# Kernel optimization log

Measured on AMD Instinct MI355X. Metric: run time of the kernel, lower is better.

The kernel has to match this reference:

```python
import jax, jax.numpy as jnp
import numpy as np
from jax import lax

B, T, E, K = 64, 512, 2048, 32


def setup_inputs() -> dict:
    key = jax.random.key(0)
    ks = jax.random.split(key, 8)
    X = jax.random.normal(ks[0], (B, T, E), dtype=jnp.float32)
    y = jax.random.randint(ks[1], (B, T), 0, K, dtype=jnp.int32)
    # variable-length mask: lengths in [T//2, T], position 0 always valid
    lengths = jax.random.randint(ks[2], (B,), T // 2, T + 1)
    mask = (jnp.arange(T)[None, :] < lengths[:, None])
    W = jax.random.normal(ks[3], (E, K), dtype=jnp.float32) * 0.02
    b = jnp.zeros((K,), dtype=jnp.float32)
    transitions = jax.random.normal(ks[4], (K, K), dtype=jnp.float32) * 0.1
    start_transitions = jax.random.normal(ks[5], (K,), dtype=jnp.float32) * 0.1
    end_transitions = jax.random.normal(ks[6], (K,), dtype=jnp.float32) * 0.1
    return {"X": X, "y": y, "mask": mask, "W": W, "b": b,
            "transitions": transitions,
            "start_transitions": start_transitions,
            "end_transitions": end_transitions}


def _input_likelihood(logits, mask, trans, start, end):
    # forward algorithm (log partition), AllenNLP semantics
    lt = jnp.transpose(logits, (1, 0, 2))  # [T,B,K]
    mt = mask.T                            # [T,B]
    alpha0 = start[None, :] + lt[0]        # [B,K]

    def step(alpha, xm):
        x, m = xm  # x:[B,K], m:[B]
        inner = alpha[:, :, None] + trans[None, :, :] + x[:, None, :]  # [B,K,K]
        new = jax.nn.logsumexp(inner, axis=1)
        return jnp.where(m[:, None], new, alpha), None

    alpha, _ = lax.scan(step, alpha0, (lt[1:], mt[1:]))
    return jax.nn.logsumexp(alpha + end[None, :], axis=1)  # [B]


def _joint_likelihood(logits, tags, mask, trans, start, end):
    maskf = mask.astype(logits.dtype)
    emit = jnp.take_along_axis(logits, tags[:, :, None], axis=2)[:, :, 0]  # [B,T]
    emit_score = jnp.sum(emit * maskf, axis=1)
    trans_sc = trans[tags[:, :-1], tags[:, 1:]]  # [B,T-1]
    trans_score = jnp.sum(trans_sc * maskf[:, 1:], axis=1)
    lengths = jnp.sum(mask.astype(jnp.int32), axis=1)
    last_tags = jnp.take_along_axis(tags, (lengths - 1)[:, None], axis=1)[:, 0]
    return start[tags[:, 0]] + emit_score + trans_score + end[last_tags]


def reference(X, y, mask, W, b, transitions, start_transitions, end_transitions):
    logits = jnp.einsum('bte,ek->btk', X, W) + b  # projection
    log_num = _joint_likelihood(logits, y, mask, transitions,
                                start_transitions, end_transitions)
    log_den = _input_likelihood(logits, mask, transitions,
                                start_transitions, end_transitions)
    # CRF.forward training path: loss = -crf(inputs, tags, mask)
    return -jnp.sum(log_num - log_den)
```

## Files before the change

### kernel.cpp

```cpp
#include <hip/hip_runtime.h>

#define Bn 64
#define Tn 512
#define En 2048
#define Kn 32
#define Mn (Bn*Tn)
#define LOG2E 1.4426950408889634f
#define LN2   0.6931471805599453f
#define NSEG 8
#define SEGLEN 64

typedef __attribute__((ext_vector_type(8)))  short short8;
typedef __attribute__((ext_vector_type(4)))  float floatx4;
typedef __attribute__((ext_vector_type(16))) float floatx16;

__device__ inline unsigned int pack_bf16(float a, float b) {
    unsigned int ua = __float_as_uint(a), ub = __float_as_uint(b);
    return ((ua + 0x8000u) >> 16) | (((ub + 0x8000u) & 0xFFFF0000u));
}
__device__ inline unsigned int pack_trunc(float lo, float hi) {
    return (__float_as_uint(lo) >> 16) | (__float_as_uint(hi) & 0xFFFF0000u);
}
__device__ inline float rdlane(float v, int l) {
    return __uint_as_float(__builtin_amdgcn_readlane(__float_as_uint(v), l));
}

__global__ __launch_bounds__(256) void prep_kernel(const float* __restrict__ W,
                                                   unsigned short* __restrict__ Wt,
                                                   float* __restrict__ out) {
    int idx = blockIdx.x * 256 + threadIdx.x;
    int k = idx >> 11, e = idx & 2047;
    float w = W[e * Kn + k];
    Wt[idx] = (unsigned short)((__float_as_uint(w) + 0x8000u) >> 16);
    if (idx == 0) out[0] = 0.f;
}

__global__ __launch_bounds__(256) void gemm_kernel(const float* __restrict__ X,
                                                   const float* __restrict__ bias,
                                                   const unsigned short* __restrict__ Wt,
                                                   float* __restrict__ logits2) {
    const int tid  = threadIdx.x;
    const int wave = tid >> 6;
    const int lane = tid & 63;
    const int ml   = lane & 15;
    const int quad = lane >> 4;
    const int row0 = blockIdx.x * 64;

    const float*          xp  = X  + (size_t)(row0 + wave * 16 + ml) * En + quad * 8;
    const unsigned short* b0p = Wt + ml * En        + quad * 8;
    const unsigned short* b1p = Wt + (16 + ml) * En + quad * 8;

    floatx4 acc0 = {0.f,0.f,0.f,0.f};
    floatx4 acc1 = {0.f,0.f,0.f,0.f};

    #pragma unroll 8
    for (int e0 = 0; e0 < En; e0 += 32) {
        float4 xa = *(const float4*)(xp + e0);
        float4 xb = *(const float4*)(xp + e0 + 4);
        short8 b0 = *(const short8*)(b0p + e0);
        short8 b1 = *(const short8*)(b1p + e0);
        union { unsigned int u[4]; short8 s; } av;
        av.u[0] = pack_bf16(xa.x, xa.y);
        av.u[1] = pack_bf16(xa.z, xa.w);
        av.u[2] = pack_bf16(xb.x, xb.y);
        av.u[3] = pack_bf16(xb.z, xb.w);
        acc0 = __builtin_amdgcn_mfma_f32_16x16x32_bf16(av.s, b0, acc0, 0, 0, 0);
        acc1 = __builtin_amdgcn_mfma_f32_16x16x32_bf16(av.s, b1, acc1, 0, 0, 0);
    }

    const float bc0 = bias[ml], bc1 = bias[16 + ml];
    const int gr = row0 + wave * 16 + quad * 4;
    #pragma unroll
    for (int r = 0; r < 4; ++r) {
        logits2[(size_t)(gr + r) * Kn + ml]      = (acc0[r] + bc0) * LOG2E;
        logits2[(size_t)(gr + r) * Kn + 16 + ml] = (acc1[r] + bc1) * LOG2E;
    }
}

__device__ inline int seq_len(const void* maskp, int b, int lane) {
    unsigned int first = *(const unsigned int*)maskp;
    int mode = (first <= 1u) ? 0 : (first == 0x3F800000u ? 2 : 1);
    int len = 0;
    if (mode == 0) {
        const int* mb = (const int*)maskp + b * Tn;
        for (int t = lane; t < Tn; t += 64) len += (mb[t] != 0);
    } else if (mode == 1) {
        const unsigned char* mb = (const unsigned char*)maskp + b * Tn;
        for (int t = lane; t < Tn; t += 64) len += (mb[t] != 0);
    } else {
        const float* mb = (const float*)maskp + b * Tn;
        for (int t = lane; t < Tn; t += 64) len += (mb[t] != 0.f);
    }
    #pragma unroll
    for (int o = 32; o; o >>= 1) len += __shfl_xor(len, o, 64);
    return len;
}

__global__ __launch_bounds__(64) void crf_seg_kernel(const float* __restrict__ logits2,
                                                     const void* __restrict__ maskp,
                                                     const float* __restrict__ trans,
                                                     float* __restrict__ Hs,
                                                     float* __restrict__ Ss) {
    const int bx = blockIdx.x;
    const int b = bx >> 3, s = bx & 7;
    const int lane = threadIdx.x;
    const int j = lane & 31;
    const int h = lane >> 5;

    const int len = seq_len(maskp, b, lane);
    if (s * SEGLEN >= len) return;
    const int tstart = (s == 0) ? 1 : s * SEGLEN;
    const int tend   = min(s * SEGLEN + SEGLEN - 1, len - 1);

    float PT1[8], PT2[8];
    #pragma unroll
    for (int i = 0; i < 8; ++i) {
        PT1[i] = __builtin_exp2f(trans[(8 * h + i) * Kn + j] * LOG2E);
        PT2[i] = __builtin_exp2f(trans[(16 + 8 * h + i) * Kn + j] * LOG2E);
    }

    union U4 { unsigned int u[4]; short8 v; };
    U4 fb1, fb2;
    #pragma unroll
    for (int p = 0; p < 4; ++p) { fb1.u[p] = 0u; fb2.u[p] = 0u; }
    int i1 = j - 8 * h;
    if (i1 >= 0 && i1 < 8) fb1.u[i1 >> 1] |= 0x3F80u << (16 * (i1 & 1));
    int i2 = j - 16 - 8 * h;
    if (i2 >= 0 && i2 < 8) fb2.u[i2 >> 1] |= 0x3F80u << (16 * (i2 & 1));

    const float* xrow = logits2 + (size_t)b * Tn * Kn + j;
    floatx16 Hc;
    float S = 0.f;
    int stepc = 0;

    float cur[4], nxt[4];
    #pragma unroll
    for (int q = 0; q < 4; ++q) cur[q] = xrow[min(tstart + q, tend) * Kn];

    for (int g = tstart; g <= tend; g += 4) {
        #pragma unroll
        for (int q = 0; q < 4; ++q) nxt[q] = xrow[min(g + 4 + q, tend) * Kn];
        #pragma unroll
        for (int q = 0; q < 4; ++q) {
            if (g + q <= tend) {
                float e = __builtin_exp2f(cur[q]);
                U4 fa1, fa2;
                #pragma unroll
                for (int p = 0; p < 4; ++p) {
                    fa1.u[p] = pack_trunc(e * PT1[2 * p], e * PT1[2 * p + 1]);
                    fa2.u[p] = pack_trunc(e * PT2[2 * p], e * PT2[2 * p + 1]);
                }
                floatx16 acc = {0.f,0.f,0.f,0.f,0.f,0.f,0.f,0.f,
                                0.f,0.f,0.f,0.f,0.f,0.f,0.f,0.f};
                acc = __builtin_amdgcn_mfma_f32_32x32x16_bf16(fa1.v, fb1.v, acc, 0, 0, 0);
                acc = __builtin_amdgcn_mfma_f32_32x32x16_bf16(fa2.v, fb2.v, acc, 0, 0, 0);

                if ((stepc & 7) == 7) {
                    float m = acc[0];
                    #pragma unroll
                    for (int r = 1; r < 16; ++r) m = fmaxf(m, acc[r]);
                    #pragma unroll
                    for (int o = 1; o < 64; o <<= 1) m = fmaxf(m, __shfl_xor(m, o, 64));
                    int eb = (int)((__float_as_uint(m) >> 23) & 0xFF);
                    float scale = __uint_as_float((unsigned int)(254 - eb) << 23);
                    #pragma unroll
                    for (int r = 0; r < 16; ++r) acc[r] *= scale;
                    S += (float)(eb - 127);
                }
                ++stepc;
                Hc = acc;

                unsigned int w[8], pw[8];
                #pragma unroll
                for (int p = 0; p < 8; ++p) w[p] = pack_trunc(acc[2 * p], acc[2 * p + 1]);
                #pragma unroll
                for (int p = 0; p < 8; ++p) pw[p] = __shfl_xor(w[p], 32, 64);
                if (h == 0) {
                    fb1.u[0] = w[0];  fb1.u[1] = w[1];  fb1.u[2] = pw[0]; fb1.u[3] = pw[1];
                    fb2.u[0] = w[4];  fb2.u[1] = w[5];  fb2.u[2] = pw[4]; fb2.u[3] = pw[5];
                } else {
                    fb1.u[0] = pw[2]; fb1.u[1] = pw[3]; fb1.u[2] = w[2];  fb1.u[3] = w[3];
                    fb2.u[0] = pw[6]; fb2.u[1] = pw[7]; fb2.u[2] = w[6];  fb2.u[3] = w[7];
                }
            }
        }
        #pragma unroll
        for (int q = 0; q < 4; ++q) cur[q] = nxt[q];
    }

    float* hp = Hs + (size_t)(b * 8 + s) * 1024;
    #pragma unroll
    for (int r = 0; r < 16; ++r) {
        int row = (r & 3) + 8 * (r >> 2) + 4 * h;
        hp[row * 32 + j] = Hc[r];
    }
    if (lane == 0) Ss[b * 8 + s] = S;
}

__global__ __launch_bounds__(64) void crf_comb_kernel(const float* __restrict__ logits2,
                                                      const int* __restrict__ y,
                                                      const void* __restrict__ maskp,
                                                      const float* __restrict__ trans,
                                                      const float* __restrict__ start,
                                                      const float* __restrict__ endt,
                                                      const float* __restrict__ Hs,
                                                      const float* __restrict__ Ss,
                                                      float* __restrict__ out) {
    const int b = blockIdx.x;
    const int lane = threadIdx.x;
    const int j = lane & 31;

    const int len = seq_len(maskp, b, lane);

    const int* yb = y + b * Tn;
    float num2 = 0.f;
    for (int t = lane; t < Tn; t += 64) {
        if (t < len) {
            int yt = yb[t];
            num2 += logits2[((size_t)b * Tn + t) * Kn + yt];
            if (t >= 1) num2 += trans[yb[t - 1] * Kn + yt] * LOG2E;
        }
    }
    if (lane == 0) num2 += (start[yb[0]] + endt[yb[len - 1]]) * LOG2E;
    #pragma unroll
    for (int o = 32; o; o >>= 1) num2 += __shfl_xor(num2, o, 64);

    float a2 = start[j] * LOG2E + logits2[(size_t)b * Tn * Kn + j];
    float m0 = a2;
    #pragma unroll
    for (int o = 1; o < 64; o <<= 1) m0 = fmaxf(m0, __shfl_xor(m0, o, 64));
    float S = m0;
    float u = __builtin_exp2f(a2 - m0);

    for (int s = 0; s < NSEG; ++s) {
        if (s * SEGLEN >= len) break;
        const float* hrow = Hs + (size_t)(b * 8 + s) * 1024 + j * 32;
        float4 hr[8];
        #pragma unroll
        for (int p = 0; p < 8; ++p) hr[p] = *(const float4*)(hrow + 4 * p);
        float v0 = 0.f, v1 = 0.f, v2 = 0.f, v3 = 0.f;
        #pragma unroll
        for (int p = 0; p < 8; ++p) {
            v0 = fmaf(hr[p].x, rdlane(u, 4 * p),     v0);
            v1 = fmaf(hr[p].y, rdlane(u, 4 * p + 1), v1);
            v2 = fmaf(hr[p].z, rdlane(u, 4 * p + 2), v2);
            v3 = fmaf(hr[p].w, rdlane(u, 4 * p + 3), v3);
        }
        float v = (v0 + v1) + (v2 + v3);
        float mm = v;
        #pragma unroll
        for (int o = 1; o < 64; o <<= 1) mm = fmaxf(mm, __shfl_xor(mm, o, 64));
        int eb = (int)((__float_as_uint(mm) >> 23) & 0xFF);
        u = v * __uint_as_float((unsigned int)(254 - eb) << 23);
        S += (float)(eb - 127) + Ss[b * 8 + s];
    }

    float fv = (lane < 32) ? u * __builtin_exp2f(endt[j] * LOG2E) : 0.f;
    #pragma unroll
    for (int o = 32; o; o >>= 1) fv += __shfl_xor(fv, o, 64);
    float den2 = S + __builtin_log2f(fv);

    if (lane == 0) atomicAdd(out, (den2 - num2) * LN2);
}

extern "C" void kernel_launch(void* const* d_in, const int* in_sizes, int n_in,
                              void* d_out, int out_size, void* d_ws, size_t ws_size,
                              hipStream_t stream) {
    const float* X     = (const float*)d_in[0];
    const int*   y     = (const int*)  d_in[1];
    const void*  mask  =               d_in[2];
    const float* W     = (const float*)d_in[3];
    const float* bias  = (const float*)d_in[4];
    const float* trans = (const float*)d_in[5];
    const float* start = (const float*)d_in[6];
    const float* endt  = (const float*)d_in[7];
    float* out = (float*)d_out;

    char* ws = (char*)d_ws;
    float*          logits2 = (float*)ws;                         ws += (size_t)Mn * Kn * 4;
    unsigned short* Wt      = (unsigned short*)ws;                ws += (size_t)Kn * En * 2;
    float*          Hs      = (float*)ws;                         ws += (size_t)Bn * NSEG * 1024 * 4;
    float*          Ss      = (float*)ws;

    prep_kernel<<<256, 256, 0, stream>>>(W, Wt, out);
    gemm_kernel<<<Mn / 64, 256, 0, stream>>>(X, bias, Wt, logits2);
    crf_seg_kernel<<<Bn * NSEG, 64, 0, stream>>>(logits2, mask, trans, Hs, Ss);
    crf_comb_kernel<<<Bn, 64, 0, stream>>>(logits2, y, mask, trans, start, endt, Hs, Ss, out);
}
```

Baseline: 431.9 us.

## Fuse projection GEMM with per-segment CRF forward scan via shared-memory logits

Merges the GEMM kernel and the segmented CRF forward kernel into one launch. Each 64-row GEMM block maps to exactly one (batch, segment) pair, keeps its logits tile in LDS, and wave 0 then runs the segment recurrence from LDS instead of rereading global memory. This removes a kernel launch and the global round-trip for the scan inputs. The cost is that the serial scan now runs on only one wave of a 256-thread block while the other waves sit idle, which may reduce GEMM occupancy or lengthen the block's tail.

```diff
diff --git a/kernel.cpp b/kernel.cpp
--- a/kernel.cpp
+++ b/kernel.cpp
@@ -33,48 +33,6 @@
     float w = W[e * Kn + k];
     Wt[idx] = (unsigned short)((__float_as_uint(w) + 0x8000u) >> 16);
     if (idx == 0) out[0] = 0.f;
-}
-
-__global__ __launch_bounds__(256) void gemm_kernel(const float* __restrict__ X,
-                                                   const float* __restrict__ bias,
-                                                   const unsigned short* __restrict__ Wt,
-                                                   float* __restrict__ logits2) {
-    const int tid  = threadIdx.x;
-    const int wave = tid >> 6;
-    const int lane = tid & 63;
-    const int ml   = lane & 15;
-    const int quad = lane >> 4;
-    const int row0 = blockIdx.x * 64;
-
-    const float*          xp  = X  + (size_t)(row0 + wave * 16 + ml) * En + quad * 8;
-    const unsigned short* b0p = Wt + ml * En        + quad * 8;
-    const unsigned short* b1p = Wt + (16 + ml) * En + quad * 8;
-
-    floatx4 acc0 = {0.f,0.f,0.f,0.f};
-    floatx4 acc1 = {0.f,0.f,0.f,0.f};
-
-    #pragma unroll 8
-    for (int e0 = 0; e0 < En; e0 += 32) {
-        float4 xa = *(const float4*)(xp + e0);
-        float4 xb = *(const float4*)(xp + e0 + 4);
-        short8 b0 = *(const short8*)(b0p + e0);
-        short8 b1 = *(const short8*)(b1p + e0);
-        union { unsigned int u[4]; short8 s; } av;
-        av.u[0] = pack_bf16(xa.x, xa.y);
-        av.u[1] = pack_bf16(xa.z, xa.w);
-        av.u[2] = pack_bf16(xb.x, xb.y);
-        av.u[3] = pack_bf16(xb.z, xb.w);
-        acc0 = __builtin_amdgcn_mfma_f32_16x16x32_bf16(av.s, b0, acc0, 0, 0, 0);
-        acc1 = __builtin_amdgcn_mfma_f32_16x16x32_bf16(av.s, b1, acc1, 0, 0, 0);
-    }
-
-    const float bc0 = bias[ml], bc1 = bias[16 + ml];
-    const int gr = row0 + wave * 16 + quad * 4;
-    #pragma unroll
-    for (int r = 0; r < 4; ++r) {
-        logits2[(size_t)(gr + r) * Kn + ml]      = (acc0[r] + bc0) * LOG2E;
-        logits2[(size_t)(gr + r) * Kn + 16 + ml] = (acc1[r] + bc1) * LOG2E;
-    }
 }
 
 __device__ inline int seq_len(const void* maskp, int b, int lane) {
@@ -96,14 +54,63 @@
     return len;
 }
 
-__global__ __launch_bounds__(64) void crf_seg_kernel(const float* __restrict__ logits2,
-                                                     const void* __restrict__ maskp,
-                                                     const float* __restrict__ trans,
-                                                     float* __restrict__ Hs,
-                                                     float* __restrict__ Ss) {
-    const int bx = blockIdx.x;
-    const int b = bx >> 3, s = bx & 7;
-    const int lane = threadIdx.x;
+__global__ __launch_bounds__(256) void gemm_seg_kernel(const float* __restrict__ X,
+                                                       const float* __restrict__ bias,
+                                                       const unsigned short* __restrict__ Wt,
+                                                       const void* __restrict__ maskp,
+                                                       const float* __restrict__ trans,
+                                                       float* __restrict__ logits2,
+                                                       float* __restrict__ Hs,
+                                                       float* __restrict__ Ss) {
+    __shared__ float sL[64][33];
+
+    const int tid  = threadIdx.x;
+    const int wave = tid >> 6;
+    const int lane = tid & 63;
+    const int ml   = lane & 15;
+    const int quad = lane >> 4;
+    const int row0 = blockIdx.x * 64;
+
+    {
+        const float*          xp  = X  + (size_t)(row0 + wave * 16 + ml) * En + quad * 8;
+        const unsigned short* b0p = Wt + ml * En        + quad * 8;
+        const unsigned short* b1p = Wt + (16 + ml) * En + quad * 8;
+
+        floatx4 acc0 = {0.f,0.f,0.f,0.f};
+        floatx4 acc1 = {0.f,0.f,0.f,0.f};
+
+        #pragma unroll 8
+        for (int e0 = 0; e0 < En; e0 += 32) {
+            float4 xa = *(const float4*)(xp + e0);
+            float4 xb = *(const float4*)(xp + e0 + 4);
+            short8 b0 = *(const short8*)(b0p + e0);
+            short8 b1 = *(const short8*)(b1p + e0);
+            union { unsigned int u[4]; short8 s; } av;
+            av.u[0] = pack_bf16(xa.x, xa.y);
+            av.u[1] = pack_bf16(xa.z, xa.w);
+            av.u[2] = pack_bf16(xb.x, xb.y);
+            av.u[3] = pack_bf16(xb.z, xb.w);
+            acc0 = __builtin_amdgcn_mfma_f32_16x16x32_bf16(av.s, b0, acc0, 0, 0, 0);
+            acc1 = __builtin_amdgcn_mfma_f32_16x16x32_bf16(av.s, b1, acc1, 0, 0, 0);
+        }
+
+        const float bc0 = bias[ml], bc1 = bias[16 + ml];
+        const int gr = row0 + wave * 16 + quad * 4;
+        const int rl = wave * 16 + quad * 4;
+        #pragma unroll
+        for (int r = 0; r < 4; ++r) {
+            float v0 = (acc0[r] + bc0) * LOG2E;
+            float v1 = (acc1[r] + bc1) * LOG2E;
+            logits2[(size_t)(gr + r) * Kn + ml]      = v0;
+            logits2[(size_t)(gr + r) * Kn + 16 + ml] = v1;
+            sL[rl + r][ml]      = v0;
+            sL[rl + r][16 + ml] = v1;
+        }
+    }
+    __syncthreads();
+    if (wave != 0) return;
+
+    const int b = blockIdx.x >> 3, s = blockIdx.x & 7;
     const int j = lane & 31;
     const int h = lane >> 5;
 
@@ -111,6 +118,8 @@
     if (s * SEGLEN >= len) return;
     const int tstart = (s == 0) ? 1 : s * SEGLEN;
     const int tend   = min(s * SEGLEN + SEGLEN - 1, len - 1);
+    const int l0   = tstart - s * SEGLEN;
+    const int lend = tend   - s * SEGLEN;
 
     float PT1[8], PT2[8];
     #pragma unroll
@@ -128,21 +137,20 @@
     int i2 = j - 16 - 8 * h;
     if (i2 >= 0 && i2 < 8) fb2.u[i2 >> 1] |= 0x3F80u << (16 * (i2 & 1));
 
-    const float* xrow = logits2 + (size_t)b * Tn * Kn + j;
     floatx16 Hc;
     float S = 0.f;
     int stepc = 0;
 
     float cur[4], nxt[4];
     #pragma unroll
-    for (int q = 0; q < 4; ++q) cur[q] = xrow[min(tstart + q, tend) * Kn];
-
-    for (int g = tstart; g <= tend; g += 4) {
-        #pragma unroll
-        for (int q = 0; q < 4; ++q) nxt[q] = xrow[min(g + 4 + q, tend) * Kn];
+    for (int q = 0; q < 4; ++q) cur[q] = sL[min(l0 + q, lend)][j];
+
+    for (int g = l0; g <= lend; g += 4) {
+        #pragma unroll
+        for (int q = 0; q < 4; ++q) nxt[q] = sL[min(g + 4 + q, lend)][j];
         #pragma unroll
         for (int q = 0; q < 4; ++q) {
-            if (g + q <= tend) {
+            if (g + q <= lend) {
                 float e = __builtin_exp2f(cur[q]);
                 U4 fa1, fa2;
                 #pragma unroll
@@ -277,13 +285,12 @@
     float* out = (float*)d_out;
 
     char* ws = (char*)d_ws;
-    float*          logits2 = (float*)ws;                         ws += (size_t)Mn * Kn * 4;
-    unsigned short* Wt      = (unsigned short*)ws;                ws += (size_t)Kn * En * 2;
-    float*          Hs      = (float*)ws;                         ws += (size_t)Bn * NSEG * 1024 * 4;
+    float*          logits2 = (float*)ws;          ws += (size_t)Mn * Kn * 4;
+    unsigned short* Wt      = (unsigned short*)ws; ws += (size_t)Kn * En * 2;
+    float*          Hs      = (float*)ws;          ws += (size_t)Bn * NSEG * 1024 * 4;
     float*          Ss      = (float*)ws;
 
     prep_kernel<<<256, 256, 0, stream>>>(W, Wt, out);
-    gemm_kernel<<<Mn / 64, 256, 0, stream>>>(X, bias, Wt, logits2);
-    crf_seg_kernel<<<Bn * NSEG, 64, 0, stream>>>(logits2, mask, trans, Hs, Ss);
+    gemm_seg_kernel<<<Mn / 64, 256, 0, stream>>>(X, bias, Wt, mask, trans, logits2, Hs, Ss);
     crf_comb_kernel<<<Bn, 64, 0, stream>>>(logits2, y, mask, trans, start, endt, Hs, Ss, out);
 }
```

New measurement: 439.0 us. No clear change (+1.6%).
